# Optimization experiments

Hardware: AMD Instinct MI355X
Metric: run time of the kernel (lower is better)

The kernel has to match this reference:

```python
import jax, jax.numpy as jnp
import numpy as np

N_NODES = 100000
N_EDGES = 1600000
HIDDEN = 64
IN_DIM = 3
OUT_DIM = 2
N_MP = 3


def setup_inputs() -> dict:
    key = jax.random.key(0)
    ks = jax.random.split(key, 16)
    x = jax.random.normal(ks[0], (N_NODES, IN_DIM), dtype=jnp.float32)
    edge_index = jax.random.randint(ks[1], (2, N_EDGES), 0, N_NODES, dtype=jnp.int64)

    def lin(k, fan_in, fan_out):
        s = 1.0 / np.sqrt(fan_in)
        return jax.random.uniform(k, (fan_out, fan_in), jnp.float32, -s, s)

    inp = {
        'x': x,
        'edge_index': edge_index,
        'preW': lin(ks[2], IN_DIM, HIDDEN),
        'preb': jnp.zeros((HIDDEN,), jnp.float32),
        'postW': lin(ks[3], HIDDEN, OUT_DIM),
        'postb': jnp.zeros((OUT_DIM,), jnp.float32),
    }
    for i in range(N_MP):
        inp[f'relW{i}'] = lin(ks[4 + 3 * i], HIDDEN, HIDDEN)
        inp[f'relb{i}'] = jnp.zeros((HIDDEN,), jnp.float32)
        inp[f'rootW{i}'] = lin(ks[5 + 3 * i], HIDDEN, HIDDEN)
    return inp


def _graph_conv(h, src, dst, relW, relb, rootW):
    # PyG GraphConv: out_i = W_rel @ (sum_{j in N(i)} h_j) + b_rel + W_root @ h_i
    agg = jax.ops.segment_sum(h[src], dst, num_segments=N_NODES)  # [N, H] scatter-add
    return agg @ relW.T + relb + h @ rootW.T


def reference(x, edge_index, preW, preb, postW, postb,
              relW0, relb0, rootW0, relW1, relb1, rootW1, relW2, relb2, rootW2):
    src, dst = edge_index[0], edge_index[1]
    # pre-MP dense
    h = jax.nn.relu(x @ preW.T + preb)
    # message passing layers (GraphConv, aggr='add'), relu after each
    for relW, relb, rootW in ((relW0, relb0, rootW0),
                              (relW1, relb1, rootW1),
                              (relW2, relb2, rootW2)):
        h = jax.nn.relu(_graph_conv(h, src, dst, relW, relb, rootW))
    # post-MP dense (activation applied to final layer too, as in source)
    out = jax.nn.relu(h @ postW.T + postb)
    return out
```

## Files before the change

kernel.cpp:

```cpp
#include <hip/hip_runtime.h>
#include <hip/hip_fp16.h>

#define N_NODES 100000
#define N_EDGES 1600000
#define HID 64

#define BSH 8
#define NBKT ((N_NODES + 255) / 256)
#define CAP 6144
#define TILE 4096

#define HSC 0.015625f
#define HSCI 64.0f

typedef _Float16 f16x8 __attribute__((ext_vector_type(8)));
typedef float f32x4 __attribute__((ext_vector_type(4)));

__global__ void __launch_bounds__(512) bucket_kernel(const int* __restrict__ src,
                                                     const int* __restrict__ dst,
                                                     int* __restrict__ bcur,
                                                     unsigned int* __restrict__ tmp) {
    __shared__ unsigned long long ed[TILE];
    __shared__ int cnt[NBKT], cnt2[NBKT], scnx[NBKT], gbase[NBKT];
    __shared__ int s[512];
    int tid = threadIdx.x;
    int bstart = blockIdx.x * TILE;
    int tcnt = N_EDGES - bstart;
    if (tcnt > TILE) tcnt = TILE;
    if (tcnt < 0) tcnt = 0;
    for (int b = tid; b < NBKT; b += 512) { cnt[b] = 0; cnt2[b] = 0; }
    __syncthreads();
    for (int i = tid; i < tcnt; i += 512) atomicAdd(&cnt[dst[bstart + i] >> BSH], 1);
    __syncthreads();
    s[tid] = (tid < NBKT) ? cnt[tid] : 0;
    __syncthreads();
    for (int off = 1; off < 512; off <<= 1) {
        int add = (tid >= off) ? s[tid - off] : 0;
        __syncthreads();
        s[tid] += add;
        __syncthreads();
    }
    if (tid < NBKT) {
        scnx[tid] = s[tid] - cnt[tid];
        gbase[tid] = tid * CAP + atomicAdd(&bcur[tid], cnt[tid]);
    }
    __syncthreads();
    for (int i = tid; i < tcnt; i += 512) {
        int e = bstart + i;
        int d = dst[e], sc = src[e];
        int b = d >> BSH;
        int pos = scnx[b] + atomicAdd(&cnt2[b], 1);
        ed[pos] = ((unsigned long long)(unsigned)d << 32) | (unsigned)sc;
    }
    __syncthreads();
    for (int i = tid; i < tcnt; i += 512) {
        unsigned long long v = ed[i];
        int d = (int)(v >> 32);
        unsigned sc = (unsigned)v;
        int b = d >> BSH;
        int idx = gbase[b] + (i - scnx[b]);
        if (idx < (b + 1) * CAP)
            tmp[idx] = ((unsigned)(d & 255) << 17) | sc;
    }
}

__global__ void __launch_bounds__(256) passb_kernel(const unsigned int* __restrict__ tmp,
                                                    const int* __restrict__ bcur,
                                                    int* __restrict__ rowp,
                                                    int* __restrict__ ssrc) {
    __shared__ int red[256];
    __shared__ int cnt[256], s[256], cur[256];
    int tid = threadIdx.x;
    int b = blockIdx.x;
    int acc = 0;
    for (int i = tid; i < b; i += 256) {
        int c = bcur[i];
        if (c > CAP) c = CAP;
        acc += c;
    }
    red[tid] = acc;
    __syncthreads();
    for (int off = 128; off >= 1; off >>= 1) {
        if (tid < off) red[tid] += red[tid + off];
        __syncthreads();
    }
    int lo = red[0];
    int ne = bcur[b];
    if (ne > CAP) ne = CAP;
    if (b == NBKT - 1 && tid == 0) rowp[N_NODES] = lo + ne;
    int lo_t = b * CAP;
    cnt[tid] = 0;
    __syncthreads();
    for (int i = tid; i < ne; i += 256) atomicAdd(&cnt[tmp[lo_t + i] >> 17], 1);
    __syncthreads();
    int v = cnt[tid];
    s[tid] = v;
    __syncthreads();
    for (int off = 1; off < 256; off <<= 1) {
        int a = (tid >= off) ? s[tid - off] : 0;
        __syncthreads();
        s[tid] += a;
        __syncthreads();
    }
    int excl = lo + s[tid] - v;
    int node = (b << BSH) + tid;
    if (node < N_NODES) rowp[node] = excl;
    cur[tid] = excl;
    __syncthreads();
    for (int i = tid; i < ne; i += 256) {
        unsigned u = tmp[lo_t + i];
        int pos = atomicAdd(&cur[u >> 17], 1);
        ssrc[pos] = (int)(u & 0x1FFFF);
    }
}

template <int PRE>
__global__ void __launch_bounds__(256) gemmt_kernel(const void* __restrict__ hx,
                                                    const float* __restrict__ preW,
                                                    const float* __restrict__ preb,
                                                    const float* __restrict__ relW,
                                                    const float* __restrict__ relb,
                                                    const float* __restrict__ rootW,
                                                    __half* __restrict__ m,
                                                    __half* __restrict__ aout) {
    __shared__ __align__(16) __half hs[128 * 64];
    __shared__ __align__(16) __half ws[128 * 64];
    __shared__ float xs[PRE ? 384 : 1];
    __shared__ float pw[PRE ? 192 : 1];
    __shared__ float pbs[PRE ? 64 : 1];
    int tid = threadIdx.x;
    int i0 = blockIdx.x * 128;

#pragma unroll
    for (int it = 0; it < 4; it++) {
        int t = it * 256 + tid;
        int row = t >> 3, c = t & 7;
        const float* wsrc = (row < 64) ? &relW[row * 64 + c * 8]
                                       : &rootW[(row - 64) * 64 + c * 8];
        float4 w0 = *(const float4*)wsrc;
        float4 w1 = *(const float4*)(wsrc + 4);
        uint4 pk;
        __half2* hp = (__half2*)&pk;
        hp[0] = __floats2half2_rn(w0.x, w0.y);
        hp[1] = __floats2half2_rn(w0.z, w0.w);
        hp[2] = __floats2half2_rn(w1.x, w1.y);
        hp[3] = __floats2half2_rn(w1.z, w1.w);
        *(uint4*)&ws[row * 64 + ((c ^ (row & 7)) << 3)] = pk;
    }
    if (PRE) {
        const float* x = (const float*)hx;
        if (tid < 192) pw[tid] = preW[tid];
        if (tid < 64) pbs[tid] = preb[tid];
        for (int t = tid; t < 384; t += 256) {
            int gi = i0 * 3 + t;
            xs[t] = (gi < N_NODES * 3) ? x[gi] : 0.f;
        }
        __syncthreads();
#pragma unroll
        for (int it = 0; it < 4; it++) {
            int t = it * 256 + tid;
            int row = t >> 3, c = t & 7;
            float v[8];
#pragma unroll
            for (int u = 0; u < 8; u++) {
                int col = c * 8 + u;
                float sv = pbs[col];
                sv = fmaf(xs[row * 3 + 0], pw[col * 3 + 0], sv);
                sv = fmaf(xs[row * 3 + 1], pw[col * 3 + 1], sv);
                sv = fmaf(xs[row * 3 + 2], pw[col * 3 + 2], sv);
                v[u] = fmaxf(sv, 0.f);
            }
            uint4 pk;
            __half2* hp = (__half2*)&pk;
            hp[0] = __floats2half2_rn(v[0], v[1]);
            hp[1] = __floats2half2_rn(v[2], v[3]);
            hp[2] = __floats2half2_rn(v[4], v[5]);
            hp[3] = __floats2half2_rn(v[6], v[7]);
            *(uint4*)&hs[row * 64 + ((c ^ (row & 7)) << 3)] = pk;
        }
    } else {
        const __half* h = (const __half*)hx;
#pragma unroll
        for (int it = 0; it < 4; it++) {
            int t = it * 256 + tid;
            int row = t >> 3, c = t & 7;
            uint4 hv = {0u, 0u, 0u, 0u};
            if (i0 + row < N_NODES) hv = *(const uint4*)(h + (long)(i0 + row) * 64 + c * 8);
            *(uint4*)&hs[row * 64 + ((c ^ (row & 7)) << 3)] = hv;
        }
    }
    __syncthreads();

    int lane = tid & 63;
    int w = tid >> 6;
    int wm = w >> 1, wn = w & 1;
    int r = lane & 15, q = lane >> 4;

    f32x4 acc[4][4];
#pragma unroll
    for (int mt = 0; mt < 4; mt++)
#pragma unroll
        for (int nt = 0; nt < 4; nt++) acc[mt][nt] = (f32x4){0.f, 0.f, 0.f, 0.f};

#pragma unroll
    for (int ks = 0; ks < 2; ks++) {
        f16x8 af[4], bf[4];
#pragma unroll
        for (int mt = 0; mt < 4; mt++) {
            int row = wm * 64 + mt * 16 + r;
            int cc = (ks * 4 + q) ^ (row & 7);
            af[mt] = *(const f16x8*)&hs[row * 64 + (cc << 3)];
        }
#pragma unroll
        for (int nt = 0; nt < 4; nt++) {
            int row = wn * 64 + nt * 16 + r;
            int cc = (ks * 4 + q) ^ (row & 7);
            bf[nt] = *(const f16x8*)&ws[row * 64 + (cc << 3)];
        }
#pragma unroll
        for (int mt = 0; mt < 4; mt++)
#pragma unroll
            for (int nt = 0; nt < 4; nt++)
                acc[mt][nt] = __builtin_amdgcn_mfma_f32_16x16x32_f16(af[mt], bf[nt],
                                                                     acc[mt][nt], 0, 0, 0);
    }

    if (wn == 0) {
#pragma unroll
        for (int mt = 0; mt < 4; mt++) {
            int nb = i0 + wm * 64 + mt * 16 + q * 4;
#pragma unroll
            for (int reg = 0; reg < 4; reg++) {
                int node = nb + reg;
                if (node >= N_NODES) continue;
#pragma unroll
                for (int nt = 0; nt < 4; nt++)
                    m[(long)node * 64 + nt * 16 + r] = __float2half(acc[mt][nt][reg]);
            }
        }
    } else {
        const float asc = PRE ? HSC : 1.0f;
        float rb[4];
#pragma unroll
        for (int nt = 0; nt < 4; nt++) rb[nt] = relb[nt * 16 + r] * HSC;
#pragma unroll
        for (int mt = 0; mt < 4; mt++) {
            int nb = i0 + wm * 64 + mt * 16 + q * 4;
#pragma unroll
            for (int reg = 0; reg < 4; reg++) {
                int node = nb + reg;
                if (node >= N_NODES) continue;
#pragma unroll
                for (int nt = 0; nt < 4; nt++)
                    aout[(long)node * 64 + nt * 16 + r] =
                        __float2half(fmaf(acc[mt][nt][reg], asc, rb[nt]));
            }
        }
    }
}

template <int FINAL>
__global__ void gather_kernel(const __half* __restrict__ m, __half* __restrict__ a,
                              const int* __restrict__ rowp, const int* __restrict__ ssrc,
                              float aggscale,
                              const float* __restrict__ postW, const float* __restrict__ postb,
                              float* __restrict__ out) {
    int lane = threadIdx.x & 63;
    int wv = (blockIdx.x * blockDim.x + threadIdx.x) >> 6;
    int pb = wv * 4;
    if (pb >= N_NODES) return;
    int n = lane >> 4;
    int g = (lane >> 3) & 1;
    int f8 = (lane & 7) << 3;
    pb = __builtin_amdgcn_readfirstlane(pb);
    int q0 = rowp[pb], q1 = rowp[pb + 1], q2 = rowp[pb + 2];
    int q3 = rowp[pb + 3], q4 = rowp[pb + 4];
    int node = pb + n;
    int r0 = (n == 0) ? q0 : (n == 1) ? q1 : (n == 2) ? q2 : q3;
    int r1 = (n == 0) ? q1 : (n == 1) ? q2 : (n == 2) ? q3 : q4;
    int nedge = r1 - r0;
    uint4 av = *(const uint4*)(a + (long)node * 64 + f8);
    float a0 = 0.f, a1 = 0.f, a2 = 0.f, a3 = 0.f, a4 = 0.f, a5 = 0.f, a6 = 0.f, a7 = 0.f;
#define ACC8(u)                                                         \
    {                                                                   \
        float2 f_;                                                      \
        f_ = __half22float2(*(__half2*)&(u).x); a0 += f_.x; a1 += f_.y; \
        f_ = __half22float2(*(__half2*)&(u).y); a2 += f_.x; a3 += f_.y; \
        f_ = __half22float2(*(__half2*)&(u).z); a4 += f_.x; a5 += f_.y; \
        f_ = __half22float2(*(__half2*)&(u).w); a6 += f_.x; a7 += f_.y; \
    }
    int ns = nedge >> 1;
    int q = 0;
    for (; q + 4 <= ns; q += 4) {
        int b0 = r0 + q * 2 + g;
        int i0 = ssrc[b0];
        int i1 = ssrc[b0 + 2];
        int i2 = ssrc[b0 + 4];
        int i3 = ssrc[b0 + 6];
        uint4 u0 = *(const uint4*)(m + (long)i0 * 64 + f8);
        uint4 u1 = *(const uint4*)(m + (long)i1 * 64 + f8);
        uint4 u2 = *(const uint4*)(m + (long)i2 * 64 + f8);
        uint4 u3 = *(const uint4*)(m + (long)i3 * 64 + f8);
        ACC8(u0); ACC8(u1); ACC8(u2); ACC8(u3);
    }
    if (q + 2 <= ns) {
        int b0 = r0 + q * 2 + g;
        int i0 = ssrc[b0];
        int i1 = ssrc[b0 + 2];
        uint4 u0 = *(const uint4*)(m + (long)i0 * 64 + f8);
        uint4 u1 = *(const uint4*)(m + (long)i1 * 64 + f8);
        ACC8(u0); ACC8(u1);
        q += 2;
    }
    if (q < ns) {
        int i0 = ssrc[r0 + q * 2 + g];
        uint4 u0 = *(const uint4*)(m + (long)i0 * 64 + f8);
        ACC8(u0);
    }
    if ((nedge & 1) && g == 0) {
        int i0 = ssrc[r0 + ns * 2];
        uint4 u0 = *(const uint4*)(m + (long)i0 * 64 + f8);
        ACC8(u0);
    }
#undef ACC8
    a0 += __shfl_xor(a0, 8, 64); a1 += __shfl_xor(a1, 8, 64);
    a2 += __shfl_xor(a2, 8, 64); a3 += __shfl_xor(a3, 8, 64);
    a4 += __shfl_xor(a4, 8, 64); a5 += __shfl_xor(a5, 8, 64);
    a6 += __shfl_xor(a6, 8, 64); a7 += __shfl_xor(a7, 8, 64);
    a0 *= aggscale; a1 *= aggscale; a2 *= aggscale; a3 *= aggscale;
    a4 *= aggscale; a5 *= aggscale; a6 *= aggscale; a7 *= aggscale;
    const __half2* ap = (const __half2*)&av;
    float2 o0 = __half22float2(ap[0]), o1 = __half22float2(ap[1]);
    float2 o2 = __half22float2(ap[2]), o3 = __half22float2(ap[3]);
    a0 = fmaxf(fmaf(o0.x, HSCI, a0), 0.f); a1 = fmaxf(fmaf(o0.y, HSCI, a1), 0.f);
    a2 = fmaxf(fmaf(o1.x, HSCI, a2), 0.f); a3 = fmaxf(fmaf(o1.y, HSCI, a3), 0.f);
    a4 = fmaxf(fmaf(o2.x, HSCI, a4), 0.f); a5 = fmaxf(fmaf(o2.y, HSCI, a5), 0.f);
    a6 = fmaxf(fmaf(o3.x, HSCI, a6), 0.f); a7 = fmaxf(fmaf(o3.y, HSCI, a7), 0.f);
    if (FINAL) {
        float4 w0 = *(const float4*)(postW + f8);
        float4 w1 = *(const float4*)(postW + f8 + 4);
        float4 w2 = *(const float4*)(postW + 64 + f8);
        float4 w3 = *(const float4*)(postW + 64 + f8 + 4);
        float p0 = a0 * w0.x + a1 * w0.y + a2 * w0.z + a3 * w0.w +
                   a4 * w1.x + a5 * w1.y + a6 * w1.z + a7 * w1.w;
        float p1 = a0 * w2.x + a1 * w2.y + a2 * w2.z + a3 * w2.w +
                   a4 * w3.x + a5 * w3.y + a6 * w3.z + a7 * w3.w;
#pragma unroll
        for (int off = 1; off <= 4; off <<= 1) {
            p0 += __shfl_xor(p0, off, 64);
            p1 += __shfl_xor(p1, off, 64);
        }
        if ((lane & 15) == 0) {
            out[(long)node * 2 + 0] = fmaxf(p0 + postb[0], 0.f);
            out[(long)node * 2 + 1] = fmaxf(p1 + postb[1], 0.f);
        }
    } else {
        if (g == 0) {
            uint4 st;
            __half2* sp = (__half2*)&st;
            sp[0] = __floats2half2_rn(a0 * HSC, a1 * HSC);
            sp[1] = __floats2half2_rn(a2 * HSC, a3 * HSC);
            sp[2] = __floats2half2_rn(a4 * HSC, a5 * HSC);
            sp[3] = __floats2half2_rn(a6 * HSC, a7 * HSC);
            *(uint4*)(a + (long)node * 64 + f8) = st;
        }
    }
}

extern "C" void kernel_launch(void* const* d_in, const int* in_sizes, int n_in,
                              void* d_out, int out_size, void* d_ws, size_t ws_size,
                              hipStream_t stream) {
    const float* x = (const float*)d_in[0];
    const int* esrc = (const int*)d_in[1];
    const int* edst = esrc + N_EDGES;
    const float* preW = (const float*)d_in[2];
    const float* preb = (const float*)d_in[3];
    const float* postW = (const float*)d_in[4];
    const float* postb = (const float*)d_in[5];
    const float* relW[3] = {(const float*)d_in[6], (const float*)d_in[9], (const float*)d_in[12]};
    const float* relb[3] = {(const float*)d_in[7], (const float*)d_in[10], (const float*)d_in[13]};
    const float* rootW[3] = {(const float*)d_in[8], (const float*)d_in[11], (const float*)d_in[14]};
    float* out = (float*)d_out;

    const size_t NF = (size_t)N_NODES * HID;
    char* p = (char*)d_ws;
    __half* hA = (__half*)p; p += NF * 2;
    __half* hB = (__half*)p; p += NF * 2;
    __half* mB = (__half*)p; p += NF * 2;
    p = (char*)(((size_t)p + 255) & ~(size_t)255);
    int* rowp = (int*)p; p += (size_t)(N_NODES + 1) * 4;
    p = (char*)(((size_t)p + 255) & ~(size_t)255);
    int* ssrc = (int*)p; p += (size_t)N_EDGES * 4;
    int* bcur = (int*)p; p += 512 * 4;
    unsigned int* tmp = (unsigned int*)hA;

    hipMemsetAsync(bcur, 0, 512 * 4, stream);
    bucket_kernel<<<(N_EDGES + TILE - 1) / TILE, 512, 0, stream>>>(esrc, edst, bcur, tmp);
    passb_kernel<<<NBKT, 256, 0, stream>>>(tmp, bcur, rowp, ssrc);

    const int GEMM_BLOCKS = (N_NODES + 127) / 128;
    const int GATHER_BLOCKS = N_NODES / 16;

    const float IS1 = 64.0f;

    gemmt_kernel<1><<<GEMM_BLOCKS, 256, 0, stream>>>(x, preW, preb, relW[0], relb[0],
                                                     rootW[0], mB, hB);
    gather_kernel<0><<<GATHER_BLOCKS, 256, 0, stream>>>(mB, hB, rowp, ssrc, 1.0f,
                                                        nullptr, nullptr, nullptr);
    gemmt_kernel<0><<<GEMM_BLOCKS, 256, 0, stream>>>(hB, nullptr, nullptr, relW[1], relb[1],
                                                     rootW[1], mB, hA);
    gather_kernel<0><<<GATHER_BLOCKS, 256, 0, stream>>>(mB, hA, rowp, ssrc, IS1,
                                                        nullptr, nullptr, nullptr);
    gemmt_kernel<0><<<GEMM_BLOCKS, 256, 0, stream>>>(hA, nullptr, nullptr, relW[2], relb[2],
                                                     rootW[2], mB, hB);
    gather_kernel<1><<<GATHER_BLOCKS, 256, 0, stream>>>(mB, hB, rowp, ssrc, IS1,
                                                        postW, postb, out);
}
```

Before: 261.4 us.

## Fuse edge bucketing with first-layer GEMM into one heterogeneous launch

Merges the edge bucketing kernel and the first pre-MLP plus GEMM kernel into one launch. The first NCHUNK blocks bucket edges and the remaining blocks compute the layer-0 transform, so the two independent stages overlap on the GPU and one launch is saved. The bucket scratch buffer moves from aliasing hA to its own workspace region so the two stages do not conflict. Fused blocks use 512 threads with dynamic shared memory, which may lower occupancy for the GEMM part.

```diff
diff --git a/kernel.cpp b/kernel.cpp
--- a/kernel.cpp
+++ b/kernel.cpp
@@ -9,6 +9,7 @@
 #define NBKT ((N_NODES + 255) / 256)
 #define CAP 6144
 #define TILE 4096
+#define NCHUNK ((N_EDGES + TILE - 1) / TILE)
 
 #define HSC 0.015625f
 #define HSCI 64.0f
@@ -16,51 +17,176 @@
 typedef _Float16 f16x8 __attribute__((ext_vector_type(8)));
 typedef float f32x4 __attribute__((ext_vector_type(4)));
 
-__global__ void __launch_bounds__(512) bucket_kernel(const int* __restrict__ src,
-                                                     const int* __restrict__ dst,
-                                                     int* __restrict__ bcur,
-                                                     unsigned int* __restrict__ tmp) {
-    __shared__ unsigned long long ed[TILE];
-    __shared__ int cnt[NBKT], cnt2[NBKT], scnx[NBKT], gbase[NBKT];
-    __shared__ int s[512];
+__global__ void __launch_bounds__(512) fused0_kernel(
+    const int* __restrict__ src, const int* __restrict__ dst,
+    int* __restrict__ bcur, unsigned int* __restrict__ tmp,
+    const float* __restrict__ x, const float* __restrict__ preW,
+    const float* __restrict__ preb, const float* __restrict__ relW,
+    const float* __restrict__ relb, const float* __restrict__ rootW,
+    __half* __restrict__ m, __half* __restrict__ aout) {
+    extern __shared__ __align__(16) char smem[];
     int tid = threadIdx.x;
-    int bstart = blockIdx.x * TILE;
-    int tcnt = N_EDGES - bstart;
-    if (tcnt > TILE) tcnt = TILE;
-    if (tcnt < 0) tcnt = 0;
-    for (int b = tid; b < NBKT; b += 512) { cnt[b] = 0; cnt2[b] = 0; }
-    __syncthreads();
-    for (int i = tid; i < tcnt; i += 512) atomicAdd(&cnt[dst[bstart + i] >> BSH], 1);
-    __syncthreads();
-    s[tid] = (tid < NBKT) ? cnt[tid] : 0;
-    __syncthreads();
-    for (int off = 1; off < 512; off <<= 1) {
-        int add = (tid >= off) ? s[tid - off] : 0;
-        __syncthreads();
-        s[tid] += add;
-        __syncthreads();
-    }
-    if (tid < NBKT) {
-        scnx[tid] = s[tid] - cnt[tid];
-        gbase[tid] = tid * CAP + atomicAdd(&bcur[tid], cnt[tid]);
-    }
-    __syncthreads();
-    for (int i = tid; i < tcnt; i += 512) {
-        int e = bstart + i;
-        int d = dst[e], sc = src[e];
-        int b = d >> BSH;
-        int pos = scnx[b] + atomicAdd(&cnt2[b], 1);
-        ed[pos] = ((unsigned long long)(unsigned)d << 32) | (unsigned)sc;
-    }
-    __syncthreads();
-    for (int i = tid; i < tcnt; i += 512) {
-        unsigned long long v = ed[i];
-        int d = (int)(v >> 32);
-        unsigned sc = (unsigned)v;
-        int b = d >> BSH;
-        int idx = gbase[b] + (i - scnx[b]);
-        if (idx < (b + 1) * CAP)
-            tmp[idx] = ((unsigned)(d & 255) << 17) | sc;
+    if (blockIdx.x < NCHUNK) {
+        unsigned long long* ed = (unsigned long long*)smem;
+        int* cnt = (int*)(smem + 32768);
+        int* cnt2 = (int*)(smem + 34368);
+        int* scnx = (int*)(smem + 35968);
+        int* gbase = (int*)(smem + 37568);
+        int* s = (int*)(smem + 39168);
+        int bstart = blockIdx.x * TILE;
+        int tcnt = N_EDGES - bstart;
+        if (tcnt > TILE) tcnt = TILE;
+        if (tcnt < 0) tcnt = 0;
+        for (int b = tid; b < NBKT; b += 512) { cnt[b] = 0; cnt2[b] = 0; }
+        __syncthreads();
+        for (int i = tid; i < tcnt; i += 512) atomicAdd(&cnt[dst[bstart + i] >> BSH], 1);
+        __syncthreads();
+        s[tid] = (tid < NBKT) ? cnt[tid] : 0;
+        __syncthreads();
+        for (int off = 1; off < 512; off <<= 1) {
+            int add = (tid >= off) ? s[tid - off] : 0;
+            __syncthreads();
+            s[tid] += add;
+            __syncthreads();
+        }
+        if (tid < NBKT) {
+            scnx[tid] = s[tid] - cnt[tid];
+            gbase[tid] = tid * CAP + atomicAdd(&bcur[tid], cnt[tid]);
+        }
+        __syncthreads();
+        for (int i = tid; i < tcnt; i += 512) {
+            int e = bstart + i;
+            int d = dst[e], sc = src[e];
+            int b = d >> BSH;
+            int pos = scnx[b] + atomicAdd(&cnt2[b], 1);
+            ed[pos] = ((unsigned long long)(unsigned)d << 32) | (unsigned)sc;
+        }
+        __syncthreads();
+        for (int i = tid; i < tcnt; i += 512) {
+            unsigned long long v = ed[i];
+            int d = (int)(v >> 32);
+            unsigned sc = (unsigned)v;
+            int b = d >> BSH;
+            int idx = gbase[b] + (i - scnx[b]);
+            if (idx < (b + 1) * CAP)
+                tmp[idx] = ((unsigned)(d & 255) << 17) | sc;
+        }
+    } else {
+        __half* hs = (__half*)smem;
+        __half* ws = (__half*)(smem + 16384);
+        float* xs = (float*)(smem + 32768);
+        float* pw = (float*)(smem + 34304);
+        float* pbs = (float*)(smem + 35072);
+        int g = blockIdx.x - NCHUNK;
+        int i0 = g * 128;
+#pragma unroll
+        for (int it = 0; it < 2; it++) {
+            int t = it * 512 + tid;
+            int row = t >> 3, c = t & 7;
+            const float* wsrc = (row < 64) ? &relW[row * 64 + c * 8]
+                                           : &rootW[(row - 64) * 64 + c * 8];
+            float4 w0 = *(const float4*)wsrc;
+            float4 w1 = *(const float4*)(wsrc + 4);
+            uint4 pk;
+            __half2* hp = (__half2*)&pk;
+            hp[0] = __floats2half2_rn(w0.x, w0.y);
+            hp[1] = __floats2half2_rn(w0.z, w0.w);
+            hp[2] = __floats2half2_rn(w1.x, w1.y);
+            hp[3] = __floats2half2_rn(w1.z, w1.w);
+            *(uint4*)&ws[row * 64 + ((c ^ (row & 7)) << 3)] = pk;
+        }
+        if (tid < 192) pw[tid] = preW[tid];
+        if (tid < 64) pbs[tid] = preb[tid];
+        if (tid < 384) {
+            int gi = i0 * 3 + tid;
+            xs[tid] = (gi < N_NODES * 3) ? x[gi] : 0.f;
+        }
+        __syncthreads();
+#pragma unroll
+        for (int it = 0; it < 2; it++) {
+            int t = it * 512 + tid;
+            int row = t >> 3, c = t & 7;
+            float v[8];
+#pragma unroll
+            for (int u = 0; u < 8; u++) {
+                int col = c * 8 + u;
+                float sv = pbs[col];
+                sv = fmaf(xs[row * 3 + 0], pw[col * 3 + 0], sv);
+                sv = fmaf(xs[row * 3 + 1], pw[col * 3 + 1], sv);
+                sv = fmaf(xs[row * 3 + 2], pw[col * 3 + 2], sv);
+                v[u] = fmaxf(sv, 0.f);
+            }
+            uint4 pk;
+            __half2* hp = (__half2*)&pk;
+            hp[0] = __floats2half2_rn(v[0], v[1]);
+            hp[1] = __floats2half2_rn(v[2], v[3]);
+            hp[2] = __floats2half2_rn(v[4], v[5]);
+            hp[3] = __floats2half2_rn(v[6], v[7]);
+            *(uint4*)&hs[row * 64 + ((c ^ (row & 7)) << 3)] = pk;
+        }
+        __syncthreads();
+        int lane = tid & 63;
+        int w = tid >> 6;
+        int wm = w >> 1, wn = w & 1;
+        int r = lane & 15, q = lane >> 4;
+        f32x4 acc[2][4];
+#pragma unroll
+        for (int mt = 0; mt < 2; mt++)
+#pragma unroll
+            for (int nt = 0; nt < 4; nt++) acc[mt][nt] = (f32x4){0.f, 0.f, 0.f, 0.f};
+#pragma unroll
+        for (int ks = 0; ks < 2; ks++) {
+            f16x8 af[2], bf[4];
+#pragma unroll
+            for (int mt = 0; mt < 2; mt++) {
+                int row = wm * 32 + mt * 16 + r;
+                int cc = (ks * 4 + q) ^ (row & 7);
+                af[mt] = *(const f16x8*)&hs[row * 64 + (cc << 3)];
+            }
+#pragma unroll
+            for (int nt = 0; nt < 4; nt++) {
+                int row = wn * 64 + nt * 16 + r;
+                int cc = (ks * 4 + q) ^ (row & 7);
+                bf[nt] = *(const f16x8*)&ws[row * 64 + (cc << 3)];
+            }
+#pragma unroll
+            for (int mt = 0; mt < 2; mt++)
+#pragma unroll
+                for (int nt = 0; nt < 4; nt++)
+                    acc[mt][nt] = __builtin_amdgcn_mfma_f32_16x16x32_f16(af[mt], bf[nt],
+                                                                         acc[mt][nt], 0, 0, 0);
+        }
+        if (wn == 0) {
+#pragma unroll
+            for (int mt = 0; mt < 2; mt++) {
+                int nb = i0 + wm * 32 + mt * 16 + q * 4;
+#pragma unroll
+                for (int reg = 0; reg < 4; reg++) {
+                    int node = nb + reg;
+                    if (node >= N_NODES) continue;
+#pragma unroll
+                    for (int nt = 0; nt < 4; nt++)
+                        m[(long)node * 64 + nt * 16 + r] = __float2half(acc[mt][nt][reg]);
+                }
+            }
+        } else {
+            float rb[4];
+#pragma unroll
+            for (int nt = 0; nt < 4; nt++) rb[nt] = relb[nt * 16 + r] * HSC;
+#pragma unroll
+            for (int mt = 0; mt < 2; mt++) {
+                int nb = i0 + wm * 32 + mt * 16 + q * 4;
+#pragma unroll
+                for (int reg = 0; reg < 4; reg++) {
+                    int node = nb + reg;
+                    if (node >= N_NODES) continue;
+#pragma unroll
+                    for (int nt = 0; nt < 4; nt++)
+                        aout[(long)node * 64 + nt * 16 + r] =
+                            __float2half(fmaf(acc[mt][nt][reg], HSC, rb[nt]));
+                }
+            }
+        }
     }
 }
 
@@ -114,10 +240,7 @@
     }
 }
 
-template <int PRE>
-__global__ void __launch_bounds__(256) gemmt_kernel(const void* __restrict__ hx,
-                                                    const float* __restrict__ preW,
-                                                    const float* __restrict__ preb,
+__global__ void __launch_bounds__(256) gemmt_kernel(const __half* __restrict__ h,
                                                     const float* __restrict__ relW,
                                                     const float* __restrict__ relb,
                                                     const float* __restrict__ rootW,
@@ -125,12 +248,8 @@
                                                     __half* __restrict__ aout) {
     __shared__ __align__(16) __half hs[128 * 64];
     __shared__ __align__(16) __half ws[128 * 64];
-    __shared__ float xs[PRE ? 384 : 1];
-    __shared__ float pw[PRE ? 192 : 1];
-    __shared__ float pbs[PRE ? 64 : 1];
     int tid = threadIdx.x;
     int i0 = blockIdx.x * 128;
-
 #pragma unroll
     for (int it = 0; it < 4; it++) {
         int t = it * 256 + tid;
@@ -147,47 +266,13 @@
         hp[3] = __floats2half2_rn(w1.z, w1.w);
         *(uint4*)&ws[row * 64 + ((c ^ (row & 7)) << 3)] = pk;
     }
-    if (PRE) {
-        const float* x = (const float*)hx;
-        if (tid < 192) pw[tid] = preW[tid];
-        if (tid < 64) pbs[tid] = preb[tid];
-        for (int t = tid; t < 384; t += 256) {
-            int gi = i0 * 3 + t;
-            xs[t] = (gi < N_NODES * 3) ? x[gi] : 0.f;
-        }
-        __syncthreads();
-#pragma unroll
-        for (int it = 0; it < 4; it++) {
-            int t = it * 256 + tid;
-            int row = t >> 3, c = t & 7;
-            float v[8];
-#pragma unroll
-            for (int u = 0; u < 8; u++) {
-                int col = c * 8 + u;
-                float sv = pbs[col];
-                sv = fmaf(xs[row * 3 + 0], pw[col * 3 + 0], sv);
-                sv = fmaf(xs[row * 3 + 1], pw[col * 3 + 1], sv);
-                sv = fmaf(xs[row * 3 + 2], pw[col * 3 + 2], sv);
-                v[u] = fmaxf(sv, 0.f);
-            }
-            uint4 pk;
-            __half2* hp = (__half2*)&pk;
-            hp[0] = __floats2half2_rn(v[0], v[1]);
-            hp[1] = __floats2half2_rn(v[2], v[3]);
-            hp[2] = __floats2half2_rn(v[4], v[5]);
-            hp[3] = __floats2half2_rn(v[6], v[7]);
-            *(uint4*)&hs[row * 64 + ((c ^ (row & 7)) << 3)] = pk;
-        }
-    } else {
-        const __half* h = (const __half*)hx;
-#pragma unroll
-        for (int it = 0; it < 4; it++) {
-            int t = it * 256 + tid;
-            int row = t >> 3, c = t & 7;
-            uint4 hv = {0u, 0u, 0u, 0u};
-            if (i0 + row < N_NODES) hv = *(const uint4*)(h + (long)(i0 + row) * 64 + c * 8);
-            *(uint4*)&hs[row * 64 + ((c ^ (row & 7)) << 3)] = hv;
-        }
+#pragma unroll
+    for (int it = 0; it < 4; it++) {
+        int t = it * 256 + tid;
+        int row = t >> 3, c = t & 7;
+        uint4 hv = {0u, 0u, 0u, 0u};
+        if (i0 + row < N_NODES) hv = *(const uint4*)(h + (long)(i0 + row) * 64 + c * 8);
+        *(uint4*)&hs[row * 64 + ((c ^ (row & 7)) << 3)] = hv;
     }
     __syncthreads();
 
@@ -195,13 +280,11 @@
     int w = tid >> 6;
     int wm = w >> 1, wn = w & 1;
     int r = lane & 15, q = lane >> 4;
-
     f32x4 acc[4][4];
 #pragma unroll
     for (int mt = 0; mt < 4; mt++)
 #pragma unroll
         for (int nt = 0; nt < 4; nt++) acc[mt][nt] = (f32x4){0.f, 0.f, 0.f, 0.f};
-
 #pragma unroll
     for (int ks = 0; ks < 2; ks++) {
         f16x8 af[4], bf[4];
@@ -224,7 +307,6 @@
                 acc[mt][nt] = __builtin_amdgcn_mfma_f32_16x16x32_f16(af[mt], bf[nt],
                                                                      acc[mt][nt], 0, 0, 0);
     }
-
     if (wn == 0) {
 #pragma unroll
         for (int mt = 0; mt < 4; mt++) {
@@ -239,7 +321,6 @@
             }
         }
     } else {
-        const float asc = PRE ? HSC : 1.0f;
         float rb[4];
 #pragma unroll
         for (int nt = 0; nt < 4; nt++) rb[nt] = relb[nt * 16 + r] * HSC;
@@ -253,7 +334,7 @@
 #pragma unroll
                 for (int nt = 0; nt < 4; nt++)
                     aout[(long)node * 64 + nt * 16 + r] =
-                        __float2half(fmaf(acc[mt][nt][reg], asc, rb[nt]));
+                        __float2half(fmaf(acc[mt][nt][reg], 1.0f, rb[nt]));
             }
         }
     }
@@ -391,28 +472,25 @@
     int* rowp = (int*)p; p += (size_t)(N_NODES + 1) * 4;
     p = (char*)(((size_t)p + 255) & ~(size_t)255);
     int* ssrc = (int*)p; p += (size_t)N_EDGES * 4;
+    p = (char*)(((size_t)p + 255) & ~(size_t)255);
+    unsigned int* tmp = (unsigned int*)p; p += (size_t)NBKT * CAP * 4;
     int* bcur = (int*)p; p += 512 * 4;
-    unsigned int* tmp = (unsigned int*)hA;
-
-    hipMemsetAsync(bcur, 0, 512 * 4, stream);
-    bucket_kernel<<<(N_EDGES + TILE - 1) / TILE, 512, 0, stream>>>(esrc, edst, bcur, tmp);
-    passb_kernel<<<NBKT, 256, 0, stream>>>(tmp, bcur, rowp, ssrc);
 
     const int GEMM_BLOCKS = (N_NODES + 127) / 128;
     const int GATHER_BLOCKS = N_NODES / 16;
-
     const float IS1 = 64.0f;
 
-    gemmt_kernel<1><<<GEMM_BLOCKS, 256, 0, stream>>>(x, preW, preb, relW[0], relb[0],
-                                                     rootW[0], mB, hB);
+    hipMemsetAsync(bcur, 0, 512 * 4, stream);
+    fused0_kernel<<<NCHUNK + GEMM_BLOCKS, 512, 41216, stream>>>(
+        esrc, edst, bcur, tmp, x, preW, preb, relW[0], relb[0], rootW[0], mB, hB);
+    passb_kernel<<<NBKT, 256, 0, stream>>>(tmp, bcur, rowp, ssrc);
+
     gather_kernel<0><<<GATHER_BLOCKS, 256, 0, stream>>>(mB, hB, rowp, ssrc, 1.0f,
                                                         nullptr, nullptr, nullptr);
-    gemmt_kernel<0><<<GEMM_BLOCKS, 256, 0, stream>>>(hB, nullptr, nullptr, relW[1], relb[1],
-                                                     rootW[1], mB, hA);
+    gemmt_kernel<<<GEMM_BLOCKS, 256, 0, stream>>>(hB, relW[1], relb[1], rootW[1], mB, hA);
     gather_kernel<0><<<GATHER_BLOCKS, 256, 0, stream>>>(mB, hA, rowp, ssrc, IS1,
                                                         nullptr, nullptr, nullptr);
-    gemmt_kernel<0><<<GEMM_BLOCKS, 256, 0, stream>>>(hA, nullptr, nullptr, relW[2], relb[2],
-                                                     rootW[2], mB, hB);
+    gemmt_kernel<<<GEMM_BLOCKS, 256, 0, stream>>>(hA, relW[2], relb[2], rootW[2], mB, hB);
     gather_kernel<1><<<GATHER_BLOCKS, 256, 0, stream>>>(mB, hB, rowp, ssrc, IS1,
                                                         postW, postb, out);
 }
```

After: 252.2 us. 3.5% less time.
